# Kernel tuning notes

Hardware: AMD Instinct MI355X
Metric: run time of the kernel (lower is better)

The kernel has to match this reference:

```python
import jax, jax.numpy as jnp
import numpy as np

N_ATOMS = 50000
N_RES = 6250
C_IN = 30
E_DIM = 12
E_BOND = 150000
E_RAD = 800000
E_RES_RAD = 400000
E_CORR = 20000


def _layer_norm(h, g, b, eps=1e-5):
    mu = h.mean(-1, keepdims=True)
    var = ((h - mu) ** 2).mean(-1, keepdims=True)
    return (h - mu) / jnp.sqrt(var + eps) * g + b


def _mlp(h, W, b, g, beta):
    # Seq(Linear, ReLU, LayerNorm, Dropout) in eval mode (dropout = identity)
    return _layer_norm(jax.nn.relu(h @ W + b), g, beta)


def _point_conv(x, pos, src, dst, W, b, g, beta, num_nodes):
    # PyG PointNetConv with add_self_loops=True, aggr='add'
    loops = jnp.arange(num_nodes)
    s = jnp.concatenate([src, loops])
    d = jnp.concatenate([dst, loops])
    msg = jnp.concatenate([x[s], pos[s] - pos[d]], axis=-1)  # [E+N, F+3]
    h = _mlp(msg, W, b, g, beta)
    return jax.ops.segment_sum(h, d, num_segments=num_nodes)


def _gcne_conv(x, edge_index, edge_attr, W, bias):
    # GCNEConv: gcn_norm with self loops, message = cat(x_j, e) @ W * norm + bias, scatter-add
    n = x.shape[0]
    loops = jnp.arange(n)
    s = jnp.concatenate([edge_index[0], loops])
    d = jnp.concatenate([edge_index[1], loops])
    w_full = jnp.ones(s.shape[0], x.dtype)
    deg = jax.ops.segment_sum(w_full, d, num_segments=n)
    dinv = jnp.where(deg > 0, deg ** -0.5, 0.0)
    norm = dinv[s] * dinv[d]
    ea = jnp.concatenate([edge_attr, jnp.zeros((n, edge_attr.shape[1]), edge_attr.dtype)], axis=0)
    msg = (jnp.concatenate([x[s], ea], axis=-1) @ W) * norm[:, None] + bias
    return jax.ops.segment_sum(msg, d, num_segments=n)


def setup_inputs():
    key = jax.random.key(0)
    ks = jax.random.split(key, 20)
    inp = {}
    inp['x'] = jax.random.normal(ks[0], (N_ATOMS, C_IN), jnp.float32)
    inp['pos'] = jax.random.uniform(ks[1], (N_ATOMS, 3), jnp.float32)
    inp['edge_attr'] = jax.random.normal(ks[2], (E_BOND, E_DIM), jnp.float32)
    inp['edge_index'] = jax.random.randint(ks[3], (2, E_BOND), 0, N_ATOMS)
    inp['rad_edge_index'] = jax.random.randint(ks[4], (2, E_RAD), 0, N_ATOMS)
    inp['res_rad_edge_index'] = jax.random.randint(ks[5], (2, E_RES_RAD), 0, N_RES)
    inp['residue_index'] = jnp.sort(jax.random.randint(ks[6], (N_ATOMS,), 0, N_RES))
    inp['src_idx'] = jax.random.randint(ks[7], (E_CORR,), 0, N_RES)
    inp['tgt_idx'] = jax.random.randint(ks[8], (E_CORR,), 0, N_RES)
    inp['y_lab'] = jax.random.randint(ks[9], (E_CORR,), 0, 2).astype(jnp.int32)
    def glorot(k, shape):
        s = (2.0 / (shape[0] + shape[1])) ** 0.5
        return jax.random.normal(k, shape, jnp.float32) * s
    # conv1 local MLP [3+C_IN -> 64]
    inp['w_pc1'] = glorot(ks[10], (C_IN + 3, 64)); inp['b_pc1'] = jnp.zeros(64)
    inp['g_pc1'] = jnp.ones(64); inp['be_pc1'] = jnp.zeros(64)
    # gcn1 weight [C_IN+E_DIM -> 64]
    inp['w_gcn'] = glorot(ks[11], (C_IN + E_DIM, 64)); inp['b_gcn'] = jnp.zeros(64)
    # atom_embed MLP [64 -> 64]
    inp['w_ae'] = glorot(ks[12], (64, 64)); inp['b_ae'] = jnp.zeros(64)
    inp['g_ae'] = jnp.ones(64); inp['be_ae'] = jnp.zeros(64)
    # res_embed MLP [64 -> 64]
    inp['w_re'] = glorot(ks[13], (64, 64)); inp['b_re'] = jnp.zeros(64)
    inp['g_re'] = jnp.ones(64); inp['be_re'] = jnp.zeros(64)
    # res_conv1 local MLP [3+64 -> 128]
    inp['w_rc'] = glorot(ks[14], (64 + 3, 128)); inp['b_rc'] = jnp.zeros(128)
    inp['g_rc'] = jnp.ones(128); inp['be_rc'] = jnp.zeros(128)
    # res_conv1 global MLP [128 -> 128]
    inp['w_rg'] = glorot(ks[15], (128, 128)); inp['b_rg'] = jnp.zeros(128)
    inp['g_rg'] = jnp.ones(128); inp['be_rg'] = jnp.zeros(128)
    return inp


def reference(x, pos, edge_attr,
              w_pc1, b_pc1, g_pc1, be_pc1,
              w_gcn, b_gcn,
              w_ae, b_ae, g_ae, be_ae,
              w_re, b_re, g_re, be_re,
              w_rc, b_rc, g_rc, be_rc,
              w_rg, b_rg, g_rg, be_rg,
              edge_index, rad_edge_index, res_rad_edge_index,
              residue_index, src_idx, tgt_idx, y_lab):
    n = x.shape[0]
    # SAModule 1: PointConv over atom radius graph, aggr='add', no global_nn
    x1 = _point_conv(x, pos, rad_edge_index[0], rad_edge_index[1],
                     w_pc1, b_pc1, g_pc1, be_pc1, n)
    # GCNEConv over bond graph
    x2 = _gcne_conv(x, edge_index, edge_attr, w_gcn, b_gcn)
    atom_x = _mlp(x1 + x2, w_ae, b_ae, g_ae, be_ae)
    # atom -> residue pooling (global_add_pool / global_mean_pool)
    res_x = jax.ops.segment_sum(atom_x, residue_index, num_segments=N_RES)
    cnt = jax.ops.segment_sum(jnp.ones(n, x.dtype), residue_index, num_segments=N_RES)
    res_pos = jax.ops.segment_sum(pos, residue_index, num_segments=N_RES) / jnp.maximum(cnt, 1.0)[:, None]
    res_x = _mlp(res_x, w_re, b_re, g_re, be_re)
    # SAModule 2: PointConv over residue radius graph with global MLP
    x3 = _point_conv(res_x, res_pos, res_rad_edge_index[0], res_rad_edge_index[1],
                     w_rc, b_rc, g_rc, be_rc, N_RES)
    x3 = _mlp(x3, w_rg, b_rg, g_rg, be_rg)
    # correspondence pairs + CosineEmbeddingLoss(reduction='none')
    x_s = x3[src_idx]
    x_t = x3[tgt_idx]
    y = (2 * y_lab - 1).astype(x.dtype)  # {0,1} -> {-1,+1}
    eps = 1e-8
    cos = (x_s * x_t).sum(-1) / (jnp.maximum(jnp.linalg.norm(x_s, axis=-1), eps) *
                                 jnp.maximum(jnp.linalg.norm(x_t, axis=-1), eps))
    unweighted = jnp.where(y == 1, 1.0 - cos, jnp.maximum(cos, 0.0))
    pos_l = jnp.where(y != 1, 0.0, y)
    neg_l = 1.0 - pos_l
    pos_w = neg_l.sum() / pos_l.sum()
    loss = jnp.mean((pos_l * pos_w + neg_l) * unweighted)
    return loss
```

## Files before the change

kernel.cpp:

```cpp
#include <hip/hip_runtime.h>
#include <math.h>

#define N_ATOMS 50000
#define N_RES 6250
#define C_IN 30
#define E_DIM 12
#define E_BOND 150000
#define E_RAD 800000
#define E_RES_RAD 400000
#define E_CORR 20000

__device__ __forceinline__ float wsum(float v) {
#pragma unroll
  for (int m = 1; m < 64; m <<= 1) v += __shfl_xor(v, m, 64);
  return v;
}

template <int K>
__global__ void rowmat64(const float* __restrict__ X, const float* __restrict__ W,
                         float* __restrict__ out, int nrows) {
  const int lane = threadIdx.x & 63;
  const int wid = (blockIdx.x * blockDim.x + threadIdx.x) >> 6;
  const int nw = (gridDim.x * blockDim.x) >> 6;
  float wcol[K];
#pragma unroll
  for (int k = 0; k < K; k++) wcol[k] = W[k * 64 + lane];
  for (int r = wid; r < nrows; r += nw) {
    float acc = 0.0f;
#pragma unroll
    for (int k = 0; k < K; k++) acc += X[(size_t)r * K + k] * wcol[k];
    out[(size_t)r * 64 + lane] = acc;
  }
}

__global__ void pc1_edge(const float* __restrict__ xw1, const float* __restrict__ pos,
                         const int* __restrict__ src, const int* __restrict__ dst,
                         const float* __restrict__ W, const float* __restrict__ b,
                         const float* __restrict__ g, const float* __restrict__ be,
                         float* __restrict__ acc) {
  const int lane = threadIdx.x & 63;
  const int wid = (blockIdx.x * blockDim.x + threadIdx.x) >> 6;
  const int nw = (gridDim.x * blockDim.x) >> 6;
  const float w0 = W[(C_IN + 0) * 64 + lane];
  const float w1 = W[(C_IN + 1) * 64 + lane];
  const float w2 = W[(C_IN + 2) * 64 + lane];
  const float bb = b[lane], gg = g[lane], eb = be[lane];
  const int total = E_RAD + N_ATOMS;
  for (int e = wid; e < total; e += nw) {
    int s, d;
    float dp0 = 0.0f, dp1 = 0.0f, dp2 = 0.0f;
    if (e < E_RAD) {
      s = __builtin_amdgcn_readfirstlane(src[e]);
      d = __builtin_amdgcn_readfirstlane(dst[e]);
      dp0 = pos[s * 3 + 0] - pos[d * 3 + 0];
      dp1 = pos[s * 3 + 1] - pos[d * 3 + 1];
      dp2 = pos[s * 3 + 2] - pos[d * 3 + 2];
    } else {
      s = d = e - E_RAD;
    }
    float h = xw1[(size_t)s * 64 + lane] + bb + dp0 * w0 + dp1 * w1 + dp2 * w2;
    h = fmaxf(h, 0.0f);
    float mu = wsum(h) * (1.0f / 64.0f);
    float c = h - mu;
    float var = wsum(c * c) * (1.0f / 64.0f);
    float v = c / sqrtf(var + 1e-5f) * gg + eb;
    atomicAdd(&acc[(size_t)d * 64 + lane], v);
  }
}

__global__ void deg_init(float* __restrict__ deg) {
  int i = blockIdx.x * blockDim.x + threadIdx.x;
  if (i < N_ATOMS) deg[i] = 1.0f;
}
__global__ void deg_count(const int* __restrict__ dst, float* __restrict__ deg) {
  int i = blockIdx.x * blockDim.x + threadIdx.x;
  if (i < E_BOND) atomicAdd(&deg[dst[i]], 1.0f);
}
__global__ void deg_inv(float* __restrict__ deg) {
  int i = blockIdx.x * blockDim.x + threadIdx.x;
  if (i < N_ATOMS) deg[i] = 1.0f / sqrtf(deg[i]);
}

__global__ void gcn_self(const float* __restrict__ xw2, const float* __restrict__ dinv,
                         const float* __restrict__ b, float* __restrict__ acc) {
  int i = blockIdx.x * blockDim.x + threadIdx.x;
  if (i < N_ATOMS * 64) {
    int n = i >> 6, lane = i & 63;
    float di = dinv[n];
    acc[i] += xw2[i] * di * di + b[lane];
  }
}

__global__ void gcn_edge(const float* __restrict__ xw2, const float* __restrict__ ea,
                         const int* __restrict__ src, const int* __restrict__ dst,
                         const float* __restrict__ W, const float* __restrict__ b,
                         const float* __restrict__ dinv, float* __restrict__ acc) {
  const int lane = threadIdx.x & 63;
  const int wid = (blockIdx.x * blockDim.x + threadIdx.x) >> 6;
  const int nw = (gridDim.x * blockDim.x) >> 6;
  float we[E_DIM];
#pragma unroll
  for (int k = 0; k < E_DIM; k++) we[k] = W[(C_IN + k) * 64 + lane];
  const float bb = b[lane];
  for (int e = wid; e < E_BOND; e += nw) {
    int s = __builtin_amdgcn_readfirstlane(src[e]);
    int d = __builtin_amdgcn_readfirstlane(dst[e]);
    float t = xw2[(size_t)s * 64 + lane];
#pragma unroll
    for (int k = 0; k < E_DIM; k++) t += ea[(size_t)e * E_DIM + k] * we[k];
    t = t * (dinv[s] * dinv[d]) + bb;
    atomicAdd(&acc[(size_t)d * 64 + lane], t);
  }
}

__global__ void atom_embed(const float* __restrict__ acc12, const float* __restrict__ pos,
                           const int* __restrict__ resid, const float* __restrict__ W,
                           const float* __restrict__ b, const float* __restrict__ g,
                           const float* __restrict__ be, float* __restrict__ res_acc,
                           float* __restrict__ res_pacc, float* __restrict__ res_cnt) {
  const int lane = threadIdx.x & 63;
  const int wid = (blockIdx.x * blockDim.x + threadIdx.x) >> 6;
  const int nw = (gridDim.x * blockDim.x) >> 6;
  const float bb = b[lane], gg = g[lane], eb = be[lane];
  for (int r = wid; r < N_ATOMS; r += nw) {
    float vin = acc12[(size_t)r * 64 + lane];
    float acc = bb;
#pragma unroll 8
    for (int k = 0; k < 64; k++) {
      float xv = __shfl(vin, k, 64);
      acc += xv * W[k * 64 + lane];
    }
    float h = fmaxf(acc, 0.0f);
    float mu = wsum(h) * (1.0f / 64.0f);
    float c = h - mu;
    float var = wsum(c * c) * (1.0f / 64.0f);
    float v = c / sqrtf(var + 1e-5f) * gg + eb;
    int rr = resid[r];
    atomicAdd(&res_acc[(size_t)rr * 64 + lane], v);
    if (lane < 3) atomicAdd(&res_pacc[rr * 3 + lane], pos[r * 3 + lane]);
    if (lane == 3) atomicAdd(&res_cnt[rr], 1.0f);
  }
}

__global__ void res_embed(const float* __restrict__ racc, const float* __restrict__ pacc,
                          const float* __restrict__ cnt, const float* __restrict__ W,
                          const float* __restrict__ b, const float* __restrict__ g,
                          const float* __restrict__ be, float* __restrict__ res_x,
                          float* __restrict__ res_pos) {
  const int lane = threadIdx.x & 63;
  const int wid = (blockIdx.x * blockDim.x + threadIdx.x) >> 6;
  const int nw = (gridDim.x * blockDim.x) >> 6;
  const float bb = b[lane], gg = g[lane], eb = be[lane];
  for (int r = wid; r < N_RES; r += nw) {
    float vin = racc[(size_t)r * 64 + lane];
    float acc = bb;
#pragma unroll 8
    for (int k = 0; k < 64; k++) {
      float xv = __shfl(vin, k, 64);
      acc += xv * W[k * 64 + lane];
    }
    float h = fmaxf(acc, 0.0f);
    float mu = wsum(h) * (1.0f / 64.0f);
    float c = h - mu;
    float var = wsum(c * c) * (1.0f / 64.0f);
    res_x[(size_t)r * 64 + lane] = c / sqrtf(var + 1e-5f) * gg + eb;
    if (lane < 3) res_pos[r * 3 + lane] = pacc[r * 3 + lane] / fmaxf(cnt[r], 1.0f);
  }
}

__global__ void rc_pre(const float* __restrict__ rx, const float* __restrict__ W,
                       const float* __restrict__ b, float* __restrict__ rw) {
  const int lane = threadIdx.x & 63;
  const int wid = (blockIdx.x * blockDim.x + threadIdx.x) >> 6;
  const int nw = (gridDim.x * blockDim.x) >> 6;
  for (int r = wid; r < N_RES; r += nw) {
    float vin = rx[(size_t)r * 64 + lane];
    float a0 = b[lane], a1 = b[64 + lane];
#pragma unroll 8
    for (int k = 0; k < 64; k++) {
      float xv = __shfl(vin, k, 64);
      a0 += xv * W[k * 128 + lane];
      a1 += xv * W[k * 128 + 64 + lane];
    }
    rw[(size_t)r * 128 + lane] = a0;
    rw[(size_t)r * 128 + 64 + lane] = a1;
  }
}

__global__ void rc_edge(const float* __restrict__ rw, const float* __restrict__ rpos,
                        const int* __restrict__ src, const int* __restrict__ dst,
                        const float* __restrict__ W, const float* __restrict__ g,
                        const float* __restrict__ be, float* __restrict__ acc) {
  const int lane = threadIdx.x & 63;
  const int wid = (blockIdx.x * blockDim.x + threadIdx.x) >> 6;
  const int nw = (gridDim.x * blockDim.x) >> 6;
  float wa[3], wb[3];
#pragma unroll
  for (int i = 0; i < 3; i++) {
    wa[i] = W[(64 + i) * 128 + lane];
    wb[i] = W[(64 + i) * 128 + 64 + lane];
  }
  const float g0 = g[lane], g1 = g[64 + lane], e0 = be[lane], e1 = be[64 + lane];
  const int total = E_RES_RAD + N_RES;
  for (int e = wid; e < total; e += nw) {
    int s, d;
    float dp0 = 0.0f, dp1 = 0.0f, dp2 = 0.0f;
    if (e < E_RES_RAD) {
      s = __builtin_amdgcn_readfirstlane(src[e]);
      d = __builtin_amdgcn_readfirstlane(dst[e]);
      dp0 = rpos[s * 3 + 0] - rpos[d * 3 + 0];
      dp1 = rpos[s * 3 + 1] - rpos[d * 3 + 1];
      dp2 = rpos[s * 3 + 2] - rpos[d * 3 + 2];
    } else {
      s = d = e - E_RES_RAD;
    }
    float h0 = rw[(size_t)s * 128 + lane] + dp0 * wa[0] + dp1 * wa[1] + dp2 * wa[2];
    float h1 = rw[(size_t)s * 128 + 64 + lane] + dp0 * wb[0] + dp1 * wb[1] + dp2 * wb[2];
    h0 = fmaxf(h0, 0.0f);
    h1 = fmaxf(h1, 0.0f);
    float mu = wsum(h0 + h1) * (1.0f / 128.0f);
    float c0 = h0 - mu, c1 = h1 - mu;
    float var = wsum(c0 * c0 + c1 * c1) * (1.0f / 128.0f);
    float rs = 1.0f / sqrtf(var + 1e-5f);
    atomicAdd(&acc[(size_t)d * 128 + lane], c0 * rs * g0 + e0);
    atomicAdd(&acc[(size_t)d * 128 + 64 + lane], c1 * rs * g1 + e1);
  }
}

__global__ void rg_embed(const float* __restrict__ acc, const float* __restrict__ W,
                         const float* __restrict__ b, const float* __restrict__ g,
                         const float* __restrict__ be, float* __restrict__ x3) {
  const int lane = threadIdx.x & 63;
  const int wid = (blockIdx.x * blockDim.x + threadIdx.x) >> 6;
  const int nw = (gridDim.x * blockDim.x) >> 6;
  for (int r = wid; r < N_RES; r += nw) {
    float i0 = acc[(size_t)r * 128 + lane];
    float i1 = acc[(size_t)r * 128 + 64 + lane];
    float a0 = b[lane], a1 = b[64 + lane];
#pragma unroll 8
    for (int k = 0; k < 64; k++) {
      float x0 = __shfl(i0, k, 64);
      float x1 = __shfl(i1, k, 64);
      a0 += x0 * W[k * 128 + lane] + x1 * W[(k + 64) * 128 + lane];
      a1 += x0 * W[k * 128 + 64 + lane] + x1 * W[(k + 64) * 128 + 64 + lane];
    }
    float h0 = fmaxf(a0, 0.0f), h1 = fmaxf(a1, 0.0f);
    float mu = wsum(h0 + h1) * (1.0f / 128.0f);
    float c0 = h0 - mu, c1 = h1 - mu;
    float var = wsum(c0 * c0 + c1 * c1) * (1.0f / 128.0f);
    float rs = 1.0f / sqrtf(var + 1e-5f);
    x3[(size_t)r * 128 + lane] = c0 * rs * g[lane] + be[lane];
    x3[(size_t)r * 128 + 64 + lane] = c1 * rs * g[64 + lane] + be[64 + lane];
  }
}

__global__ void loss_pairs(const float* __restrict__ x3, const int* __restrict__ si,
                           const int* __restrict__ ti, const int* __restrict__ y,
                           float* __restrict__ lacc) {
  const int lane = threadIdx.x & 63;
  const int wid = (blockIdx.x * blockDim.x + threadIdx.x) >> 6;
  const int nw = (gridDim.x * blockDim.x) >> 6;
  float sp = 0.0f, sn = 0.0f, cp = 0.0f, cn = 0.0f;
  for (int p = wid; p < E_CORR; p += nw) {
    int a = si[p], bI = ti[p], yy = y[p];
    float a0 = x3[(size_t)a * 128 + lane], a1 = x3[(size_t)a * 128 + 64 + lane];
    float b0 = x3[(size_t)bI * 128 + lane], b1 = x3[(size_t)bI * 128 + 64 + lane];
    float dot = wsum(a0 * b0 + a1 * b1);
    float na = wsum(a0 * a0 + a1 * a1);
    float nb = wsum(b0 * b0 + b1 * b1);
    float cosv = dot / (fmaxf(sqrtf(na), 1e-8f) * fmaxf(sqrtf(nb), 1e-8f));
    if (yy == 1) {
      sp += 1.0f - cosv;
      cp += 1.0f;
    } else {
      sn += fmaxf(cosv, 0.0f);
      cn += 1.0f;
    }
  }
  if (lane == 0) {
    atomicAdd(&lacc[0], sp);
    atomicAdd(&lacc[1], sn);
    atomicAdd(&lacc[2], cp);
    atomicAdd(&lacc[3], cn);
  }
}

__global__ void finalize(const float* __restrict__ lacc, float* __restrict__ out) {
  if (blockIdx.x == 0 && threadIdx.x == 0) {
    float pw = lacc[3] / lacc[2];
    out[0] = (lacc[0] * pw + lacc[1]) / (float)E_CORR;
  }
}

extern "C" void kernel_launch(void* const* d_in, const int* in_sizes, int n_in,
                              void* d_out, int out_size, void* d_ws, size_t ws_size,
                              hipStream_t stream) {
  const float* x = (const float*)d_in[0];
  const float* pos = (const float*)d_in[1];
  const float* edge_attr = (const float*)d_in[2];
  const int* edge_index = (const int*)d_in[3];
  const int* rad_ei = (const int*)d_in[4];
  const int* res_rad_ei = (const int*)d_in[5];
  const int* resid = (const int*)d_in[6];
  const int* src_idx = (const int*)d_in[7];
  const int* tgt_idx = (const int*)d_in[8];
  const int* y_lab = (const int*)d_in[9];
  const float* w_pc1 = (const float*)d_in[10];
  const float* b_pc1 = (const float*)d_in[11];
  const float* g_pc1 = (const float*)d_in[12];
  const float* be_pc1 = (const float*)d_in[13];
  const float* w_gcn = (const float*)d_in[14];
  const float* b_gcn = (const float*)d_in[15];
  const float* w_ae = (const float*)d_in[16];
  const float* b_ae = (const float*)d_in[17];
  const float* g_ae = (const float*)d_in[18];
  const float* be_ae = (const float*)d_in[19];
  const float* w_re = (const float*)d_in[20];
  const float* b_re = (const float*)d_in[21];
  const float* g_re = (const float*)d_in[22];
  const float* be_re = (const float*)d_in[23];
  const float* w_rc = (const float*)d_in[24];
  const float* b_rc = (const float*)d_in[25];
  const float* g_rc = (const float*)d_in[26];
  const float* be_rc = (const float*)d_in[27];
  const float* w_rg = (const float*)d_in[28];
  const float* b_rg = (const float*)d_in[29];
  const float* g_rg = (const float*)d_in[30];
  const float* be_rg = (const float*)d_in[31];

  float* ws = (float*)d_ws;
  float* acc12 = ws;
  float* res_acc = acc12 + (size_t)N_ATOMS * 64;
  float* res_pacc = res_acc + (size_t)N_RES * 64;
  float* res_cnt = res_pacc + 18752;
  float* x3acc = res_cnt + 6272;
  float* lacc = x3acc + (size_t)N_RES * 128;
  size_t zero_floats = (size_t)N_ATOMS * 64 + (size_t)N_RES * 64 + 18752 + 6272 +
                       (size_t)N_RES * 128 + 8;
  float* xw1 = lacc + 8;
  float* xw2 = xw1 + (size_t)N_ATOMS * 64;
  float* deg = xw2 + (size_t)N_ATOMS * 64;
  float* res_x = deg + N_ATOMS;
  float* res_pos = res_x + (size_t)N_RES * 64;
  float* rw = res_pos + 18752;
  float* x3 = rw + (size_t)N_RES * 128;

  hipMemsetAsync(d_ws, 0, zero_floats * sizeof(float), stream);

  const int B = 256;
  const int GB = 2048;
  const int GS = 512;

  rowmat64<C_IN><<<GB, B, 0, stream>>>(x, w_pc1, xw1, N_ATOMS);
  pc1_edge<<<GB, B, 0, stream>>>(xw1, pos, rad_ei, rad_ei + E_RAD, w_pc1, b_pc1, g_pc1,
                                 be_pc1, acc12);

  deg_init<<<(N_ATOMS + B - 1) / B, B, 0, stream>>>(deg);
  deg_count<<<(E_BOND + B - 1) / B, B, 0, stream>>>(edge_index + E_BOND, deg);
  deg_inv<<<(N_ATOMS + B - 1) / B, B, 0, stream>>>(deg);

  rowmat64<C_IN><<<GB, B, 0, stream>>>(x, w_gcn, xw2, N_ATOMS);
  gcn_self<<<(N_ATOMS * 64 + B - 1) / B, B, 0, stream>>>(xw2, deg, b_gcn, acc12);
  gcn_edge<<<GB, B, 0, stream>>>(xw2, edge_attr, edge_index, edge_index + E_BOND, w_gcn,
                                 b_gcn, deg, acc12);

  atom_embed<<<GB, B, 0, stream>>>(acc12, pos, resid, w_ae, b_ae, g_ae, be_ae, res_acc,
                                   res_pacc, res_cnt);

  res_embed<<<GS, B, 0, stream>>>(res_acc, res_pacc, res_cnt, w_re, b_re, g_re, be_re,
                                  res_x, res_pos);

  rc_pre<<<GS, B, 0, stream>>>(res_x, w_rc, b_rc, rw);
  rc_edge<<<GB, B, 0, stream>>>(rw, res_pos, res_rad_ei, res_rad_ei + E_RES_RAD, w_rc,
                                g_rc, be_rc, x3acc);
  rg_embed<<<GS, B, 0, stream>>>(x3acc, w_rg, b_rg, g_rg, be_rg, x3);

  loss_pairs<<<GS, B, 0, stream>>>(x3, src_idx, tgt_idx, y_lab, lacc);
  finalize<<<1, 64, 0, stream>>>(lacc, (float*)d_out);
}
```

Baseline: 789.1 us.

## Process two edges per wave, single-pass layernorm stats, fold GCN self-loop into embed

The point-conv edge kernels now handle two edges per wavefront iteration, so more independent gathers and atomics are in flight at once. Layernorm mean and variance are computed in one fused shuffle reduction using E[x^2]-mu^2 with rsqrt, in place of two sequential reductions and a division. The separate gcn_self kernel is removed and its self-loop term is folded into atom_embed's input read, saving a full read-modify-write pass over the atom accumulator. The loss kernel reduces its three sums in one loop with wave-uniform indices. The one-pass variance formula may be slightly less numerically accurate.

```diff
diff --git a/kernel.cpp b/kernel.cpp
--- a/kernel.cpp
+++ b/kernel.cpp
@@ -10,6 +10,8 @@
 #define E_RES_RAD 400000
 #define E_CORR 20000
 
+__device__ __forceinline__ int rfl(int v) { return __builtin_amdgcn_readfirstlane(v); }
+
 __device__ __forceinline__ float wsum(float v) {
 #pragma unroll
   for (int m = 1; m < 64; m <<= 1) v += __shfl_xor(v, m, 64);
@@ -46,25 +48,46 @@
   const float w2 = W[(C_IN + 2) * 64 + lane];
   const float bb = b[lane], gg = g[lane], eb = be[lane];
   const int total = E_RAD + N_ATOMS;
-  for (int e = wid; e < total; e += nw) {
-    int s, d;
-    float dp0 = 0.0f, dp1 = 0.0f, dp2 = 0.0f;
-    if (e < E_RAD) {
-      s = __builtin_amdgcn_readfirstlane(src[e]);
-      d = __builtin_amdgcn_readfirstlane(dst[e]);
-      dp0 = pos[s * 3 + 0] - pos[d * 3 + 0];
-      dp1 = pos[s * 3 + 1] - pos[d * 3 + 1];
-      dp2 = pos[s * 3 + 2] - pos[d * 3 + 2];
+  for (int e0 = wid * 2; e0 < total; e0 += nw * 2) {
+    const int e1 = e0 + 1;
+    int sA, dA, sB, dB;
+    float dA0 = 0.0f, dA1 = 0.0f, dA2 = 0.0f, dB0 = 0.0f, dB1 = 0.0f, dB2 = 0.0f;
+    if (e0 < E_RAD) {
+      sA = rfl(src[e0]); dA = rfl(dst[e0]);
+      dA0 = pos[sA * 3 + 0] - pos[dA * 3 + 0];
+      dA1 = pos[sA * 3 + 1] - pos[dA * 3 + 1];
+      dA2 = pos[sA * 3 + 2] - pos[dA * 3 + 2];
     } else {
-      s = d = e - E_RAD;
-    }
-    float h = xw1[(size_t)s * 64 + lane] + bb + dp0 * w0 + dp1 * w1 + dp2 * w2;
-    h = fmaxf(h, 0.0f);
-    float mu = wsum(h) * (1.0f / 64.0f);
-    float c = h - mu;
-    float var = wsum(c * c) * (1.0f / 64.0f);
-    float v = c / sqrtf(var + 1e-5f) * gg + eb;
-    atomicAdd(&acc[(size_t)d * 64 + lane], v);
+      sA = dA = e0 - E_RAD;
+    }
+    if (e1 < E_RAD) {
+      sB = rfl(src[e1]); dB = rfl(dst[e1]);
+      dB0 = pos[sB * 3 + 0] - pos[dB * 3 + 0];
+      dB1 = pos[sB * 3 + 1] - pos[dB * 3 + 1];
+      dB2 = pos[sB * 3 + 2] - pos[dB * 3 + 2];
+    } else {
+      sB = dB = e1 - E_RAD;
+    }
+    float hA = xw1[(size_t)sA * 64 + lane] + bb + dA0 * w0 + dA1 * w1 + dA2 * w2;
+    float hB = xw1[(size_t)sB * 64 + lane] + bb + dB0 * w0 + dB1 * w1 + dB2 * w2;
+    hA = fmaxf(hA, 0.0f);
+    hB = fmaxf(hB, 0.0f);
+    float s1A = hA, s2A = hA * hA, s1B = hB, s2B = hB * hB;
+#pragma unroll
+    for (int m = 1; m < 64; m <<= 1) {
+      s1A += __shfl_xor(s1A, m, 64);
+      s2A += __shfl_xor(s2A, m, 64);
+      s1B += __shfl_xor(s1B, m, 64);
+      s2B += __shfl_xor(s2B, m, 64);
+    }
+    const float muA = s1A * (1.0f / 64.0f);
+    const float muB = s1B * (1.0f / 64.0f);
+    const float vaA = s2A * (1.0f / 64.0f) - muA * muA;
+    const float vaB = s2B * (1.0f / 64.0f) - muB * muB;
+    const float rA = rsqrtf(vaA + 1e-5f);
+    const float rB = rsqrtf(vaB + 1e-5f);
+    atomicAdd(&acc[(size_t)dA * 64 + lane], (hA - muA) * rA * gg + eb);
+    atomicAdd(&acc[(size_t)dB * 64 + lane], (hB - muB) * rB * gg + eb);
   }
 }
 
@@ -78,17 +101,7 @@
 }
 __global__ void deg_inv(float* __restrict__ deg) {
   int i = blockIdx.x * blockDim.x + threadIdx.x;
-  if (i < N_ATOMS) deg[i] = 1.0f / sqrtf(deg[i]);
-}
-
-__global__ void gcn_self(const float* __restrict__ xw2, const float* __restrict__ dinv,
-                         const float* __restrict__ b, float* __restrict__ acc) {
-  int i = blockIdx.x * blockDim.x + threadIdx.x;
-  if (i < N_ATOMS * 64) {
-    int n = i >> 6, lane = i & 63;
-    float di = dinv[n];
-    acc[i] += xw2[i] * di * di + b[lane];
-  }
+  if (i < N_ATOMS) deg[i] = rsqrtf(deg[i]);
 }
 
 __global__ void gcn_edge(const float* __restrict__ xw2, const float* __restrict__ ea,
@@ -103,8 +116,8 @@
   for (int k = 0; k < E_DIM; k++) we[k] = W[(C_IN + k) * 64 + lane];
   const float bb = b[lane];
   for (int e = wid; e < E_BOND; e += nw) {
-    int s = __builtin_amdgcn_readfirstlane(src[e]);
-    int d = __builtin_amdgcn_readfirstlane(dst[e]);
+    int s = rfl(src[e]);
+    int d = rfl(dst[e]);
     float t = xw2[(size_t)s * 64 + lane];
 #pragma unroll
     for (int k = 0; k < E_DIM; k++) t += ea[(size_t)e * E_DIM + k] * we[k];
@@ -113,17 +126,20 @@
   }
 }
 
-__global__ void atom_embed(const float* __restrict__ acc12, const float* __restrict__ pos,
-                           const int* __restrict__ resid, const float* __restrict__ W,
-                           const float* __restrict__ b, const float* __restrict__ g,
-                           const float* __restrict__ be, float* __restrict__ res_acc,
-                           float* __restrict__ res_pacc, float* __restrict__ res_cnt) {
-  const int lane = threadIdx.x & 63;
-  const int wid = (blockIdx.x * blockDim.x + threadIdx.x) >> 6;
-  const int nw = (gridDim.x * blockDim.x) >> 6;
-  const float bb = b[lane], gg = g[lane], eb = be[lane];
+__global__ void atom_embed(const float* __restrict__ acc12, const float* __restrict__ xw2,
+                           const float* __restrict__ dinv, const float* __restrict__ bgcn,
+                           const float* __restrict__ pos, const int* __restrict__ resid,
+                           const float* __restrict__ W, const float* __restrict__ b,
+                           const float* __restrict__ g, const float* __restrict__ be,
+                           float* __restrict__ res_acc, float* __restrict__ res_pacc,
+                           float* __restrict__ res_cnt) {
+  const int lane = threadIdx.x & 63;
+  const int wid = (blockIdx.x * blockDim.x + threadIdx.x) >> 6;
+  const int nw = (gridDim.x * blockDim.x) >> 6;
+  const float bb = b[lane], gg = g[lane], eb = be[lane], bg = bgcn[lane];
   for (int r = wid; r < N_ATOMS; r += nw) {
-    float vin = acc12[(size_t)r * 64 + lane];
+    const float di = dinv[r];
+    float vin = acc12[(size_t)r * 64 + lane] + xw2[(size_t)r * 64 + lane] * di * di + bg;
     float acc = bb;
 #pragma unroll 8
     for (int k = 0; k < 64; k++) {
@@ -131,10 +147,15 @@
       acc += xv * W[k * 64 + lane];
     }
     float h = fmaxf(acc, 0.0f);
-    float mu = wsum(h) * (1.0f / 64.0f);
-    float c = h - mu;
-    float var = wsum(c * c) * (1.0f / 64.0f);
-    float v = c / sqrtf(var + 1e-5f) * gg + eb;
+    float s1 = h, s2 = h * h;
+#pragma unroll
+    for (int m = 1; m < 64; m <<= 1) {
+      s1 += __shfl_xor(s1, m, 64);
+      s2 += __shfl_xor(s2, m, 64);
+    }
+    float mu = s1 * (1.0f / 64.0f);
+    float var = s2 * (1.0f / 64.0f) - mu * mu;
+    float v = (h - mu) * rsqrtf(var + 1e-5f) * gg + eb;
     int rr = resid[r];
     atomicAdd(&res_acc[(size_t)rr * 64 + lane], v);
     if (lane < 3) atomicAdd(&res_pacc[rr * 3 + lane], pos[r * 3 + lane]);
@@ -160,10 +181,15 @@
       acc += xv * W[k * 64 + lane];
     }
     float h = fmaxf(acc, 0.0f);
-    float mu = wsum(h) * (1.0f / 64.0f);
-    float c = h - mu;
-    float var = wsum(c * c) * (1.0f / 64.0f);
-    res_x[(size_t)r * 64 + lane] = c / sqrtf(var + 1e-5f) * gg + eb;
+    float s1 = h, s2 = h * h;
+#pragma unroll
+    for (int m = 1; m < 64; m <<= 1) {
+      s1 += __shfl_xor(s1, m, 64);
+      s2 += __shfl_xor(s2, m, 64);
+    }
+    float mu = s1 * (1.0f / 64.0f);
+    float var = s2 * (1.0f / 64.0f) - mu * mu;
+    res_x[(size_t)r * 64 + lane] = (h - mu) * rsqrtf(var + 1e-5f) * gg + eb;
     if (lane < 3) res_pos[r * 3 + lane] = pacc[r * 3 + lane] / fmaxf(cnt[r], 1.0f);
   }
 }
@@ -200,30 +226,53 @@
     wa[i] = W[(64 + i) * 128 + lane];
     wb[i] = W[(64 + i) * 128 + 64 + lane];
   }
-  const float g0 = g[lane], g1 = g[64 + lane], e0 = be[lane], e1 = be[64 + lane];
+  const float g0 = g[lane], g1 = g[64 + lane], e0c = be[lane], e1c = be[64 + lane];
   const int total = E_RES_RAD + N_RES;
-  for (int e = wid; e < total; e += nw) {
-    int s, d;
-    float dp0 = 0.0f, dp1 = 0.0f, dp2 = 0.0f;
-    if (e < E_RES_RAD) {
-      s = __builtin_amdgcn_readfirstlane(src[e]);
-      d = __builtin_amdgcn_readfirstlane(dst[e]);
-      dp0 = rpos[s * 3 + 0] - rpos[d * 3 + 0];
-      dp1 = rpos[s * 3 + 1] - rpos[d * 3 + 1];
-      dp2 = rpos[s * 3 + 2] - rpos[d * 3 + 2];
+  for (int e0 = wid * 2; e0 < total; e0 += nw * 2) {
+    const int e1 = e0 + 1;
+    int sA, dA, sB, dB;
+    float dA0 = 0.0f, dA1 = 0.0f, dA2 = 0.0f, dB0 = 0.0f, dB1 = 0.0f, dB2 = 0.0f;
+    if (e0 < E_RES_RAD) {
+      sA = rfl(src[e0]); dA = rfl(dst[e0]);
+      dA0 = rpos[sA * 3 + 0] - rpos[dA * 3 + 0];
+      dA1 = rpos[sA * 3 + 1] - rpos[dA * 3 + 1];
+      dA2 = rpos[sA * 3 + 2] - rpos[dA * 3 + 2];
     } else {
-      s = d = e - E_RES_RAD;
-    }
-    float h0 = rw[(size_t)s * 128 + lane] + dp0 * wa[0] + dp1 * wa[1] + dp2 * wa[2];
-    float h1 = rw[(size_t)s * 128 + 64 + lane] + dp0 * wb[0] + dp1 * wb[1] + dp2 * wb[2];
-    h0 = fmaxf(h0, 0.0f);
-    h1 = fmaxf(h1, 0.0f);
-    float mu = wsum(h0 + h1) * (1.0f / 128.0f);
-    float c0 = h0 - mu, c1 = h1 - mu;
-    float var = wsum(c0 * c0 + c1 * c1) * (1.0f / 128.0f);
-    float rs = 1.0f / sqrtf(var + 1e-5f);
-    atomicAdd(&acc[(size_t)d * 128 + lane], c0 * rs * g0 + e0);
-    atomicAdd(&acc[(size_t)d * 128 + 64 + lane], c1 * rs * g1 + e1);
+      sA = dA = e0 - E_RES_RAD;
+    }
+    if (e1 < E_RES_RAD) {
+      sB = rfl(src[e1]); dB = rfl(dst[e1]);
+      dB0 = rpos[sB * 3 + 0] - rpos[dB * 3 + 0];
+      dB1 = rpos[sB * 3 + 1] - rpos[dB * 3 + 1];
+      dB2 = rpos[sB * 3 + 2] - rpos[dB * 3 + 2];
+    } else {
+      sB = dB = e1 - E_RES_RAD;
+    }
+    float hA0 = rw[(size_t)sA * 128 + lane]      + dA0 * wa[0] + dA1 * wa[1] + dA2 * wa[2];
+    float hA1 = rw[(size_t)sA * 128 + 64 + lane] + dA0 * wb[0] + dA1 * wb[1] + dA2 * wb[2];
+    float hB0 = rw[(size_t)sB * 128 + lane]      + dB0 * wa[0] + dB1 * wa[1] + dB2 * wa[2];
+    float hB1 = rw[(size_t)sB * 128 + 64 + lane] + dB0 * wb[0] + dB1 * wb[1] + dB2 * wb[2];
+    hA0 = fmaxf(hA0, 0.0f); hA1 = fmaxf(hA1, 0.0f);
+    hB0 = fmaxf(hB0, 0.0f); hB1 = fmaxf(hB1, 0.0f);
+    float s1A = hA0 + hA1, s2A = hA0 * hA0 + hA1 * hA1;
+    float s1B = hB0 + hB1, s2B = hB0 * hB0 + hB1 * hB1;
+#pragma unroll
+    for (int m = 1; m < 64; m <<= 1) {
+      s1A += __shfl_xor(s1A, m, 64);
+      s2A += __shfl_xor(s2A, m, 64);
+      s1B += __shfl_xor(s1B, m, 64);
+      s2B += __shfl_xor(s2B, m, 64);
+    }
+    const float muA = s1A * (1.0f / 128.0f);
+    const float muB = s1B * (1.0f / 128.0f);
+    const float vaA = s2A * (1.0f / 128.0f) - muA * muA;
+    const float vaB = s2B * (1.0f / 128.0f) - muB * muB;
+    const float rsA = rsqrtf(vaA + 1e-5f);
+    const float rsB = rsqrtf(vaB + 1e-5f);
+    atomicAdd(&acc[(size_t)dA * 128 + lane],      (hA0 - muA) * rsA * g0 + e0c);
+    atomicAdd(&acc[(size_t)dA * 128 + 64 + lane], (hA1 - muA) * rsA * g1 + e1c);
+    atomicAdd(&acc[(size_t)dB * 128 + lane],      (hB0 - muB) * rsB * g0 + e0c);
+    atomicAdd(&acc[(size_t)dB * 128 + 64 + lane], (hB1 - muB) * rsB * g1 + e1c);
   }
 }
 
@@ -245,12 +294,17 @@
       a1 += x0 * W[k * 128 + 64 + lane] + x1 * W[(k + 64) * 128 + 64 + lane];
     }
     float h0 = fmaxf(a0, 0.0f), h1 = fmaxf(a1, 0.0f);
-    float mu = wsum(h0 + h1) * (1.0f / 128.0f);
-    float c0 = h0 - mu, c1 = h1 - mu;
-    float var = wsum(c0 * c0 + c1 * c1) * (1.0f / 128.0f);
-    float rs = 1.0f / sqrtf(var + 1e-5f);
-    x3[(size_t)r * 128 + lane] = c0 * rs * g[lane] + be[lane];
-    x3[(size_t)r * 128 + 64 + lane] = c1 * rs * g[64 + lane] + be[64 + lane];
+    float s1 = h0 + h1, s2 = h0 * h0 + h1 * h1;
+#pragma unroll
+    for (int m = 1; m < 64; m <<= 1) {
+      s1 += __shfl_xor(s1, m, 64);
+      s2 += __shfl_xor(s2, m, 64);
+    }
+    float mu = s1 * (1.0f / 128.0f);
+    float var = s2 * (1.0f / 128.0f) - mu * mu;
+    float rs = rsqrtf(var + 1e-5f);
+    x3[(size_t)r * 128 + lane] = (h0 - mu) * rs * g[lane] + be[lane];
+    x3[(size_t)r * 128 + 64 + lane] = (h1 - mu) * rs * g[64 + lane] + be[64 + lane];
   }
 }
 
@@ -262,12 +316,18 @@
   const int nw = (gridDim.x * blockDim.x) >> 6;
   float sp = 0.0f, sn = 0.0f, cp = 0.0f, cn = 0.0f;
   for (int p = wid; p < E_CORR; p += nw) {
-    int a = si[p], bI = ti[p], yy = y[p];
+    int a = rfl(si[p]), bI = rfl(ti[p]), yy = rfl(y[p]);
     float a0 = x3[(size_t)a * 128 + lane], a1 = x3[(size_t)a * 128 + 64 + lane];
     float b0 = x3[(size_t)bI * 128 + lane], b1 = x3[(size_t)bI * 128 + 64 + lane];
-    float dot = wsum(a0 * b0 + a1 * b1);
-    float na = wsum(a0 * a0 + a1 * a1);
-    float nb = wsum(b0 * b0 + b1 * b1);
+    float dot = a0 * b0 + a1 * b1;
+    float na = a0 * a0 + a1 * a1;
+    float nb = b0 * b0 + b1 * b1;
+#pragma unroll
+    for (int m = 1; m < 64; m <<= 1) {
+      dot += __shfl_xor(dot, m, 64);
+      na += __shfl_xor(na, m, 64);
+      nb += __shfl_xor(nb, m, 64);
+    }
     float cosv = dot / (fmaxf(sqrtf(na), 1e-8f) * fmaxf(sqrtf(nb), 1e-8f));
     if (yy == 1) {
       sp += 1.0f - cosv;
@@ -360,12 +420,11 @@
   deg_inv<<<(N_ATOMS + B - 1) / B, B, 0, stream>>>(deg);
 
   rowmat64<C_IN><<<GB, B, 0, stream>>>(x, w_gcn, xw2, N_ATOMS);
-  gcn_self<<<(N_ATOMS * 64 + B - 1) / B, B, 0, stream>>>(xw2, deg, b_gcn, acc12);
   gcn_edge<<<GB, B, 0, stream>>>(xw2, edge_attr, edge_index, edge_index + E_BOND, w_gcn,
                                  b_gcn, deg, acc12);
 
-  atom_embed<<<GB, B, 0, stream>>>(acc12, pos, resid, w_ae, b_ae, g_ae, be_ae, res_acc,
-                                   res_pacc, res_cnt);
+  atom_embed<<<GB, B, 0, stream>>>(acc12, xw2, deg, b_gcn, pos, resid, w_ae, b_ae, g_ae,
+                                   be_ae, res_acc, res_pacc, res_cnt);
 
   res_embed<<<GS, B, 0, stream>>>(res_acc, res_pacc, res_cnt, w_re, b_re, g_re, be_re,
                                   res_x, res_pos);
```

Result: faster. 772.9 us (-2.0%).
